# Kernel optimization log

Measured on AMD Instinct MI355X. Metric: run time of the kernel, lower is better.

## Reference

```python
import jax, jax.numpy as jnp
import numpy as np

# Shapes hard-coded by the original module
B, C1, C2, S, K, H, E = 128, 128, 14, 14, 3, 256, 2  # batch, chan-split, chan-split, spatial, kernel, hidden, expand


def setup_inputs() -> dict:
    key = jax.random.key(0)
    k1, k2, k3 = jax.random.split(key, 3)
    x = jax.random.normal(k1, (B, C1 * C2, S), dtype=jnp.float32)
    w0 = jax.random.normal(k2, (H, E), dtype=jnp.float32)        # weights[0]
    w1 = jax.random.normal(k3, (C1, K, H), dtype=jnp.float32)    # weights[1]
    return {"x": x, "w0": w0, "w1": w1, "shift": 1}


def reference(x, w0, w1, shift):
    # reshape to (B, C1, C2, S); original torch treats it as (B, 1792, 14, 1)
    xr = x.reshape(B, C1, C2, S)
    # unfold((3,1), padding=(1,0)): 1D im2col along the S (=14) axis
    xp = jnp.pad(xr, ((0, 0), (0, 0), (0, 0), (1, 1)))
    # patches[b, j, n, i, m] = xp[b, j, n, m + i]  -> (B, C1, C2, K, S)
    patches = jnp.stack([xp[..., k:k + S] for k in range(K)], axis=3)
    # einsum 'ljnmi,jik->lnmk' (torch had m,i swapped via permute; fold it in)
    t4 = jnp.einsum('ljnim,jik->lnmk', patches, w1)   # (B, C2, S, H)
    # einsum 'kmlj,ji->kmlji': outer product with w0 along a new expand dim
    t5 = t4[..., None] * w0                            # (B, C2, S, H, E)
    t5 = jnp.roll(t5, shift, axis=1)                   # cyclic shift over C2
    t6 = jnp.transpose(t5, (0, 2, 3, 1, 4)).reshape(B, S, H, C2 * E)
    t6 = jnp.roll(t6, shift, axis=3)                   # cyclic shift over merged (C2*E)
    t6 = t6.reshape(B, S, H, C2, E).sum(axis=4)        # (B, S, H, C2)
    return jnp.transpose(t6, (0, 2, 3, 1))             # (B, H, C2, S) = (128, 256, 14, 14)
```

## Files before the change

kernel.cpp:

```cpp
#include <hip/hip_runtime.h>
#include <hip/hip_bf16.h>
#include <math.h>

#define B_   128
#define C1_  128
#define C2_  14
#define S_   14
#define K_   3
#define H_   256
#define E_   2

#define HT   64
#define NT   4
#define XROWS 224
#define BT_OFF 28928
#define CROW 228

typedef unsigned short u16;
typedef unsigned int   u32;
typedef __attribute__((ext_vector_type(8))) short bf16x8;
typedef __attribute__((ext_vector_type(4))) float f32x4;

#define ASYNC16(g, l) __builtin_amdgcn_global_load_lds(                        \
    (const __attribute__((address_space(1))) void*)(g),                        \
    (__attribute__((address_space(3))) void*)(l), 16, 0, 0)

__device__ __forceinline__ u16 f2bf(float f) {
    u32 u = __float_as_uint(f);
    return (u16)((u + 0x7FFF + ((u >> 16) & 1)) >> 16);
}

__device__ __forceinline__ int decode_shift(const int* p) {
    int a = p[0];
    if (a >= -100 && a <= 100 && a != 0) return a;
    float f = __int_as_float(a);
    if (f >= -100.f && f <= 100.f && f == truncf(f) && f != 0.f) return (int)f;
    long long bits = ((long long)p[1] << 32) | (unsigned int)a;
    double d = __longlong_as_double(bits);
    if (d >= -100.0 && d <= 100.0 && d == trunc(d) && d != 0.0) return (int)d;
    return a;
}

__global__ __launch_bounds__(256) void cvt_kernel(const float* __restrict__ x,
                                                  const float* __restrict__ w1,
                                                  u16* __restrict__ xg,
                                                  u16* __restrict__ wg) {
    const int blk = blockIdx.x;
    const int t   = threadIdx.x;
    if (blk < 1024) {
        __shared__ u16 xl[64 * 50];
        const int b   = blk >> 3;
        const int hf  = (blk >> 2) & 1;
        const int qr  = blk & 3;
        const int cs0 = qr * 49;
        const float* xb = x + (size_t)(b * C1_ + hf * 64) * 196 + cs0;
#pragma unroll
        for (int i = 0; i < 13; ++i) {
            int idx = t + 256 * i;
            if (idx < 3136) {
                int c1l = idx / 49, j = idx - c1l * 49;
                xl[c1l * 50 + j] = f2bf(xb[c1l * 196 + j]);
            }
        }
        __syncthreads();
        u16* dst = xg + (size_t)(b * 2 + hf) * (XROWS * 64) + (size_t)qr * 56 * 64;
#pragma unroll
        for (int i = 0; i < 2; ++i) {
            int task = t + 256 * i;
            if (task < 448) {
                int rr = task >> 3, o = task & 7;
                int row = qr * 56 + rr;
                int p = row & 15;
                uint4 val = make_uint4(0, 0, 0, 0);
                if (p >= 1 && p <= 14) {
                    int csl = (row >> 4) * 14 + p - 1 - cs0;
                    u16 v[8];
#pragma unroll
                    for (int j = 0; j < 8; ++j) v[j] = xl[(o * 8 + j) * 50 + csl];
                    val.x = (u32)v[0] | ((u32)v[1] << 16);
                    val.y = (u32)v[2] | ((u32)v[3] << 16);
                    val.z = (u32)v[4] | ((u32)v[5] << 16);
                    val.w = (u32)v[6] | ((u32)v[7] << 16);
                }
                int op = o ^ (row & 7);
                *(uint4*)&dst[rr * 64 + op * 8] = val;
            }
        }
    } else {
        int q = (blk - 1024) * 256 + t;
        float4 v = ((const float4*)w1)[q];
        int i0 = q * 4;
        int c1 = i0 / 768;
        int kk = (i0 - c1 * 768) >> 8;
        int h0 = i0 & 255;
        int hf = c1 >> 6, c1l = c1 & 63;
        int cb0 = c1l >> 3, j = c1l & 7;
        u16 b4[4] = { f2bf(v.x), f2bf(v.y), f2bf(v.z), f2bf(v.w) };
#pragma unroll
        for (int d = 0; d < 4; ++d) {
            int h = h0 + d, g = h >> 6, hl = h & 63;
            int cb = cb0 ^ (hl & 7);
            wg[(size_t)((g * 2 + hf) * 64 + hl) * 192 + kk * 64 + cb * 8 + j] = b4[d];
        }
    }
}

__global__ __launch_bounds__(256, 2) void fused_kernel(const u16* __restrict__ xg,
                                                       const float* __restrict__ w0,
                                                       const u16* __restrict__ wg,
                                                       const int* __restrict__ shift_p,
                                                       float* __restrict__ out) {
    __shared__ __align__(16) char lds[58368];
    float* Cl = (float*)lds;

    const int raw  = blockIdx.x;
    const int xcd  = raw & 7;
    const int slot = raw >> 3;
    const int b    = xcd * 16 + (slot & 15);
    const int g    = slot >> 4;
    const int h0   = g * HT;
    const int t    = threadIdx.x;
    const int wave = t >> 6;
    const int lane = t & 63;
    const int quad = lane >> 4;
    const int l15  = lane & 15;
    const int wbase = t & ~63;

    f32x4 acc[4][NT];
#pragma unroll
    for (int i = 0; i < 4; ++i)
#pragma unroll
        for (int j = 0; j < NT; ++j) acc[i][j] = (f32x4){0.f, 0.f, 0.f, 0.f};

    for (int hf = 0; hf < 2; ++hf) {
        if (hf) __syncthreads();
        const uint4* xs = (const uint4*)(xg + (size_t)(b * 2 + hf) * (XROWS * 64));
        const uint4* bs = (const uint4*)(wg + (size_t)(g * 2 + hf) * (64 * 192));
#pragma unroll
        for (int i = 0; i < 7; ++i)
            ASYNC16(xs + 256 * i + t, lds + (size_t)(256 * i + wbase) * 16);
#pragma unroll
        for (int i = 0; i < 6; ++i)
            ASYNC16(bs + 256 * i + t, lds + BT_OFF + (size_t)(256 * i + wbase) * 16);
        __syncthreads();

#pragma unroll
        for (int tt = 0; tt < 6; ++tt) {
            const int kk  = tt >> 1;
            const int cbl = (tt & 1) * 4 + quad;
            const int bsw = (cbl ^ (l15 & 7)) << 4;
            const int asw = (cbl ^ ((l15 + kk) & 7)) << 4;
            bf16x8 bfr[NT];
#pragma unroll
            for (int nc = 0; nc < NT; ++nc)
                bfr[nc] = *(const bf16x8*)(lds + BT_OFF +
                            (nc * 16 + l15) * 384 + kk * 128 + bsw);
#pragma unroll
            for (int mi = 0; mi < 4; ++mi) {
                int mt = wave + mi * 4;
                if (mt < 14) {
                    int row = mt * 16 + l15 + kk;
                    bf16x8 af = *(const bf16x8*)(lds + row * 128 + asw);
#pragma unroll
                    for (int nc = 0; nc < NT; ++nc)
                        acc[mi][nc] = __builtin_amdgcn_mfma_f32_16x16x32_bf16(
                            af, bfr[nc], acc[mi][nc], 0, 0, 0);
                }
            }
        }
    }

    __syncthreads();
#pragma unroll
    for (int mi = 0; mi < 4; ++mi) {
        int mt = wave + mi * 4;
        if (mt < 14) {
#pragma unroll
            for (int nc = 0; nc < NT; ++nc) {
                int hl = nc * 16 + l15;
                *(f32x4*)&Cl[hl * CROW + mt * 16 + quad * 4] = acc[mi][nc];
            }
        }
    }
    __syncthreads();

    const int shift = decode_shift(shift_p);
    const int hl = t >> 2, sub = t & 3;
    const int h = h0 + hl;
    int c0[2]; float wv[2];
#pragma unroll
    for (int e = 0; e < 2; ++e) {
        int q = (e - shift) % 28; if (q < 0) q += 28;
        int np0 = q >> 1, ep = q & 1;
        int c = (np0 - shift) % 14; if (c < 0) c += 14;
        c0[e] = c;
        wv[e] = w0[h * 2 + ep];
    }
    const float* Crow = &Cl[hl * CROW];
    float* orow = out + (size_t)(b * H_ + h) * 196;
#pragma unroll
    for (int jj = 0; jj < 13; ++jj) {
        int i = sub + 4 * jj;
        if (i < 49) {
            float tmp[4];
#pragma unroll
            for (int e4 = 0; e4 < 4; ++e4) {
                int idx = 4 * i + e4;
                int n = idx / 14, m = idx - n * 14;
                int cA = c0[0] + n; if (cA >= 14) cA -= 14;
                int cB = c0[1] + n; if (cB >= 14) cB -= 14;
                tmp[e4] = wv[0] * Crow[cA * 16 + m] + wv[1] * Crow[cB * 16 + m];
            }
            *(float4*)&orow[4 * i] = make_float4(tmp[0], tmp[1], tmp[2], tmp[3]);
        }
    }
}

__global__ __launch_bounds__(256) void t4_fb(const float* __restrict__ x,
                                             const float* __restrict__ w1,
                                             float* __restrict__ t4) {
    __shared__ float xl[C1_][16];
    const int b = blockIdx.x / C2_, c2 = blockIdx.x % C2_, h = threadIdx.x;
    for (int i = h; i < C1_ * S_; i += 256) {
        int c1 = i / S_, s = i % S_;
        xl[c1][s + 1] = x[((size_t)(b * C1_ + c1) * C2_ + c2) * S_ + s];
    }
    if (h < C1_) { xl[h][0] = 0.f; xl[h][15] = 0.f; }
    __syncthreads();
    float acc[S_];
#pragma unroll
    for (int s = 0; s < S_; ++s) acc[s] = 0.f;
    for (int c1 = 0; c1 < C1_; ++c1) {
        float wa = w1[(size_t)(c1 * K_ + 0) * H_ + h];
        float wb = w1[(size_t)(c1 * K_ + 1) * H_ + h];
        float wc = w1[(size_t)(c1 * K_ + 2) * H_ + h];
#pragma unroll
        for (int s = 0; s < S_; ++s)
            acc[s] += wa * xl[c1][s] + wb * xl[c1][s + 1] + wc * xl[c1][s + 2];
    }
    size_t base = ((size_t)(b * H_ + h) * C2_ + c2) * S_;
#pragma unroll
    for (int s = 0; s < S_; ++s) t4[base + s] = acc[s];
}
__global__ __launch_bounds__(224) void out_fb(float* __restrict__ t4,
                                              const float* __restrict__ w0,
                                              const int* __restrict__ shift_p) {
    const int tid = threadIdx.x;
    const int m = tid % S_, hh = tid / S_;
    const int b = blockIdx.x / 16, h = (blockIdx.x % 16) * 16 + hh;
    const int shift = decode_shift(shift_p);
    const size_t colbase = ((size_t)(b * H_ + h) * C2_) * S_ + m;
    float tl[C2_];
#pragma unroll
    for (int c2 = 0; c2 < C2_; ++c2) tl[c2] = t4[colbase + (size_t)c2 * S_];
    const float w0v[2] = { w0[h * 2 + 0], w0[h * 2 + 1] };
    float r[C2_];
#pragma unroll
    for (int n = 0; n < C2_; ++n) {
        float a = 0.f;
#pragma unroll
        for (int e = 0; e < 2; ++e) {
            int q = (2 * n + e - shift) % 28; if (q < 0) q += 28;
            int np = q >> 1, ep = q & 1;
            int c2 = (np - shift) % 14; if (c2 < 0) c2 += 14;
            a += tl[c2] * w0v[ep];
        }
        r[n] = a;
    }
#pragma unroll
    for (int n = 0; n < C2_; ++n) t4[colbase + (size_t)n * S_] = r[n];
}

extern "C" void kernel_launch(void* const* d_in, const int* in_sizes, int n_in,
                              void* d_out, int out_size, void* d_ws, size_t ws_size,
                              hipStream_t stream) {
    const float* x     = (const float*)d_in[0];
    const float* w0    = (const float*)d_in[1];
    const float* w1    = (const float*)d_in[2];
    const int*   shift = (const int*)(n_in > 3 ? d_in[3] : d_in[n_in - 1]);
    for (int i = 0; i < n_in; ++i) {
        int sz = in_sizes[i];
        if (sz == B_ * C1_ * C2_ * S_)      x     = (const float*)d_in[i];
        else if (sz == H_ * E_)             w0    = (const float*)d_in[i];
        else if (sz == C1_ * K_ * H_)       w1    = (const float*)d_in[i];
        else if (sz == 1)                   shift = (const int*)d_in[i];
    }
    float* out = (float*)d_out;

    const size_t NXG = (size_t)B_ * 2 * XROWS * 64;
    const size_t NWG = (size_t)4 * 2 * 64 * 192;
    if (ws_size >= (NXG + NWG) * sizeof(u16)) {
        u16* xg = (u16*)d_ws;
        u16* wg = xg + NXG;
        cvt_kernel<<<1024 + 96, 256, 0, stream>>>(x, w1, xg, wg);
        fused_kernel<<<B_ * 4, 256, 0, stream>>>(xg, w0, wg, shift, out);
    } else {
        t4_fb<<<B_ * C2_, 256, 0, stream>>>(x, w1, out);
        out_fb<<<B_ * 16, 224, 0, stream>>>(out, w0, shift);
    }
}
```

Measured before the change: 90.57 us.

## Pack x rows without per-c2 padding and split fused GEMM over c2 halves

The bf16 im2col buffer drops from 16 padded rows per c2 to 15 rows, and each (b, hf) buffer is split into two 7-channel halves. The fused kernel now runs 1024 blocks that each cover one c2 half with a smaller LDS footprint, raising occupancy to 4 blocks per CU. The epilogue is rewritten to emit contiguous float2 pairs using a precomputed rotation offset. The conversion kernel is restructured to read x with float4 loads across 512-thread blocks. In exchange the B-matrix tile is loaded twice as often overall, and the output indexing is more intricate.

```diff
diff --git a/kernel.cpp b/kernel.cpp
--- a/kernel.cpp
+++ b/kernel.cpp
@@ -12,9 +12,11 @@
 
 #define HT   64
 #define NT   4
-#define XROWS 224
-#define BT_OFF 28928
-#define CROW 228
+#define XR    121
+#define XCHUNK (XR * 64)
+#define BT_OFF 15488
+#define LDS_SZ 40064
+#define CROW 116
 
 typedef unsigned short u16;
 typedef unsigned int   u32;
@@ -41,53 +43,56 @@
     return a;
 }
 
-__global__ __launch_bounds__(256) void cvt_kernel(const float* __restrict__ x,
+__global__ __launch_bounds__(512) void cvt_kernel(const float* __restrict__ x,
                                                   const float* __restrict__ w1,
                                                   u16* __restrict__ xg,
                                                   u16* __restrict__ wg) {
     const int blk = blockIdx.x;
     const int t   = threadIdx.x;
-    if (blk < 1024) {
-        __shared__ u16 xl[64 * 50];
-        const int b   = blk >> 3;
-        const int hf  = (blk >> 2) & 1;
-        const int qr  = blk & 3;
-        const int cs0 = qr * 49;
-        const float* xb = x + (size_t)(b * C1_ + hf * 64) * 196 + cs0;
-#pragma unroll
-        for (int i = 0; i < 13; ++i) {
-            int idx = t + 256 * i;
-            if (idx < 3136) {
-                int c1l = idx / 49, j = idx - c1l * 49;
-                xl[c1l * 50 + j] = f2bf(xb[c1l * 196 + j]);
+    if (blk < 256) {
+        __shared__ u16 xl[64 * 200];
+        const int b  = blk >> 1;
+        const int hf = blk & 1;
+        const float4* src = (const float4*)(x + (size_t)(b * C1_ + hf * 64) * 196);
+#pragma unroll
+        for (int i = 0; i < 7; ++i) {
+            int q = t + 512 * i;
+            if (q < 3136) {
+                float4 v = src[q];
+                int c1l = q / 49, f4 = q - c1l * 49;
+                uint2 w;
+                w.x = (u32)f2bf(v.x) | ((u32)f2bf(v.y) << 16);
+                w.y = (u32)f2bf(v.z) | ((u32)f2bf(v.w) << 16);
+                *(uint2*)&xl[c1l * 200 + f4 * 4] = w;
             }
         }
         __syncthreads();
-        u16* dst = xg + (size_t)(b * 2 + hf) * (XROWS * 64) + (size_t)qr * 56 * 64;
-#pragma unroll
-        for (int i = 0; i < 2; ++i) {
-            int task = t + 256 * i;
-            if (task < 448) {
-                int rr = task >> 3, o = task & 7;
-                int row = qr * 56 + rr;
-                int p = row & 15;
+        u16* dst = xg + (size_t)(b * 2 + hf) * (2 * XCHUNK);
+#pragma unroll
+        for (int i = 0; i < 4; ++i) {
+            int idx = t + 512 * i;
+            if (idx < 1936) {
+                int half = idx / 968, rem = idx - half * 968;
+                int rr = rem >> 3, o = rem & 7;
+                int c2l = rr / 15, p = rr - c2l * 15;
                 uint4 val = make_uint4(0, 0, 0, 0);
-                if (p >= 1 && p <= 14) {
-                    int csl = (row >> 4) * 14 + p - 1 - cs0;
+                if (p != 0 && rr != 120) {
+                    int c2g = half * 7 + c2l; if (c2g >= 14) c2g -= 14;
+                    int cs = c2g * 14 + p - 1;
                     u16 v[8];
 #pragma unroll
-                    for (int j = 0; j < 8; ++j) v[j] = xl[(o * 8 + j) * 50 + csl];
+                    for (int j = 0; j < 8; ++j) v[j] = xl[(o * 8 + j) * 200 + cs];
                     val.x = (u32)v[0] | ((u32)v[1] << 16);
                     val.y = (u32)v[2] | ((u32)v[3] << 16);
                     val.z = (u32)v[4] | ((u32)v[5] << 16);
                     val.w = (u32)v[6] | ((u32)v[7] << 16);
                 }
-                int op = o ^ (row & 7);
-                *(uint4*)&dst[rr * 64 + op * 8] = val;
+                int op = o ^ (rr & 7);
+                *(uint4*)&dst[(half * XR + rr) * 64 + op * 8] = val;
             }
         }
     } else {
-        int q = (blk - 1024) * 256 + t;
+        int q = (blk - 256) * 512 + t;
         float4 v = ((const float4*)w1)[q];
         int i0 = q * 4;
         int c1 = i0 / 768;
@@ -105,19 +110,20 @@
     }
 }
 
-__global__ __launch_bounds__(256, 2) void fused_kernel(const u16* __restrict__ xg,
+__global__ __launch_bounds__(256, 4) void fused_kernel(const u16* __restrict__ xg,
                                                        const float* __restrict__ w0,
                                                        const u16* __restrict__ wg,
                                                        const int* __restrict__ shift_p,
                                                        float* __restrict__ out) {
-    __shared__ __align__(16) char lds[58368];
+    __shared__ __align__(16) char lds[LDS_SZ];
     float* Cl = (float*)lds;
 
     const int raw  = blockIdx.x;
-    const int xcd  = raw & 7;
-    const int slot = raw >> 3;
-    const int b    = xcd * 16 + (slot & 15);
-    const int g    = slot >> 4;
+    const int u    = raw & 255;
+    const int g    = raw >> 8;
+    const int b    = u >> 1;
+    const int half = u & 1;
+    const int c0   = half * 7;
     const int h0   = g * HT;
     const int t    = threadIdx.x;
     const int wave = t >> 6;
@@ -126,19 +132,32 @@
     const int l15  = lane & 15;
     const int wbase = t & ~63;
 
-    f32x4 acc[4][NT];
-#pragma unroll
-    for (int i = 0; i < 4; ++i)
+    int rb[2]; bool vm[2];
+#pragma unroll
+    for (int mi = 0; mi < 2; ++mi) {
+        int mt = wave + 4 * mi;
+        vm[mi] = (mt < 7);
+        int m = mt * 16 + l15;
+        if (m > 111) m = 111;
+        rb[mi] = m + m / 14;
+    }
+
+    f32x4 acc[2][NT];
+#pragma unroll
+    for (int i = 0; i < 2; ++i)
 #pragma unroll
         for (int j = 0; j < NT; ++j) acc[i][j] = (f32x4){0.f, 0.f, 0.f, 0.f};
 
     for (int hf = 0; hf < 2; ++hf) {
         if (hf) __syncthreads();
-        const uint4* xs = (const uint4*)(xg + (size_t)(b * 2 + hf) * (XROWS * 64));
+        const uint4* xs = (const uint4*)(xg + ((size_t)(b * 2 + hf) * 2 + half) * XCHUNK);
         const uint4* bs = (const uint4*)(wg + (size_t)(g * 2 + hf) * (64 * 192));
 #pragma unroll
-        for (int i = 0; i < 7; ++i)
-            ASYNC16(xs + 256 * i + t, lds + (size_t)(256 * i + wbase) * 16);
+        for (int i = 0; i < 4; ++i) {
+            int idx = t + 256 * i;
+            if (idx < 968)
+                ASYNC16(xs + idx, lds + (size_t)(256 * i + wbase) * 16);
+        }
 #pragma unroll
         for (int i = 0; i < 6; ++i)
             ASYNC16(bs + 256 * i + t, lds + BT_OFF + (size_t)(256 * i + wbase) * 16);
@@ -149,18 +168,17 @@
             const int kk  = tt >> 1;
             const int cbl = (tt & 1) * 4 + quad;
             const int bsw = (cbl ^ (l15 & 7)) << 4;
-            const int asw = (cbl ^ ((l15 + kk) & 7)) << 4;
             bf16x8 bfr[NT];
 #pragma unroll
             for (int nc = 0; nc < NT; ++nc)
                 bfr[nc] = *(const bf16x8*)(lds + BT_OFF +
                             (nc * 16 + l15) * 384 + kk * 128 + bsw);
 #pragma unroll
-            for (int mi = 0; mi < 4; ++mi) {
-                int mt = wave + mi * 4;
-                if (mt < 14) {
-                    int row = mt * 16 + l15 + kk;
-                    bf16x8 af = *(const bf16x8*)(lds + row * 128 + asw);
+            for (int mi = 0; mi < 2; ++mi) {
+                if (vm[mi]) {
+                    int row = rb[mi] + kk;
+                    bf16x8 af = *(const bf16x8*)(lds + row * 128 +
+                                 ((cbl ^ (row & 7)) << 4));
 #pragma unroll
                     for (int nc = 0; nc < NT; ++nc)
                         acc[mi][nc] = __builtin_amdgcn_mfma_f32_16x16x32_bf16(
@@ -172,9 +190,9 @@
 
     __syncthreads();
 #pragma unroll
-    for (int mi = 0; mi < 4; ++mi) {
-        int mt = wave + mi * 4;
-        if (mt < 14) {
+    for (int mi = 0; mi < 2; ++mi) {
+        int mt = wave + 4 * mi;
+        if (vm[mi]) {
 #pragma unroll
             for (int nc = 0; nc < NT; ++nc) {
                 int hl = nc * 16 + l15;
@@ -187,31 +205,32 @@
     const int shift = decode_shift(shift_p);
     const int hl = t >> 2, sub = t & 3;
     const int h = h0 + hl;
-    int c0[2]; float wv[2];
+    int aE[2], epE[2];
 #pragma unroll
     for (int e = 0; e < 2; ++e) {
         int q = (e - shift) % 28; if (q < 0) q += 28;
-        int np0 = q >> 1, ep = q & 1;
-        int c = (np0 - shift) % 14; if (c < 0) c += 14;
-        c0[e] = c;
-        wv[e] = w0[h * 2 + ep];
-    }
+        int np0 = q >> 1; epE[e] = q & 1;
+        int c2p0 = (np0 - shift) % 14; if (c2p0 < 0) c2p0 += 14;
+        aE[e] = (14 - c2p0) % 14;
+    }
+    int diff = aE[0] - aE[1]; if (diff < 0) diff += 14;
+    int A = (diff == 13) ? aE[1] : aE[0];
+    int base0 = ((A - aE[0] + 14) % 14) * 14;
+    int base1 = ((A - aE[1] + 14) % 14) * 14;
+    float wv0 = w0[h * 2 + epE[0]], wv1 = w0[h * 2 + epE[1]];
+    int n0g = c0 + A; if (n0g >= 14) n0g -= 14;
+    const int o0 = n0g * 14;
     const float* Crow = &Cl[hl * CROW];
     float* orow = out + (size_t)(b * H_ + h) * 196;
 #pragma unroll
-    for (int jj = 0; jj < 13; ++jj) {
-        int i = sub + 4 * jj;
-        if (i < 49) {
-            float tmp[4];
-#pragma unroll
-            for (int e4 = 0; e4 < 4; ++e4) {
-                int idx = 4 * i + e4;
-                int n = idx / 14, m = idx - n * 14;
-                int cA = c0[0] + n; if (cA >= 14) cA -= 14;
-                int cB = c0[1] + n; if (cB >= 14) cB -= 14;
-                tmp[e4] = wv[0] * Crow[cA * 16 + m] + wv[1] * Crow[cB * 16 + m];
-            }
-            *(float4*)&orow[4 * i] = make_float4(tmp[0], tmp[1], tmp[2], tmp[3]);
+    for (int i = 0; i < 13; ++i) {
+        int j = sub + 4 * i;
+        if (j < 49) {
+            int p = 2 * j;
+            float v0 = wv0 * Crow[base0 + p]     + wv1 * Crow[base1 + p];
+            float v1 = wv0 * Crow[base0 + p + 1] + wv1 * Crow[base1 + p + 1];
+            int o = o0 + p; if (o >= 196) o -= 196;
+            *(float2*)&orow[o] = make_float2(v0, v1);
         }
     }
 }
@@ -287,13 +306,13 @@
     }
     float* out = (float*)d_out;
 
-    const size_t NXG = (size_t)B_ * 2 * XROWS * 64;
+    const size_t NXG = (size_t)B_ * 2 * 2 * XCHUNK;
     const size_t NWG = (size_t)4 * 2 * 64 * 192;
     if (ws_size >= (NXG + NWG) * sizeof(u16)) {
         u16* xg = (u16*)d_ws;
         u16* wg = xg + NXG;
-        cvt_kernel<<<1024 + 96, 256, 0, stream>>>(x, w1, xg, wg);
-        fused_kernel<<<B_ * 4, 256, 0, stream>>>(xg, w0, wg, shift, out);
+        cvt_kernel<<<304, 512, 0, stream>>>(x, w1, xg, wg);
+        fused_kernel<<<1024, 256, 0, stream>>>(xg, w0, wg, shift, out);
     } else {
         t4_fb<<<B_ * C2_, 256, 0, stream>>>(x, w1, out);
         out_fb<<<B_ * 16, 224, 0, stream>>>(out, w0, shift);
```

Measured after the change: 87.97 us (median of 2 runs). 1.03x faster.
